# Kernel optimization log

Measured on AMD Instinct MI355X. Metric: run time of the kernel, lower is better.

Reference implementation:

```python
import jax, jax.numpy as jnp
import numpy as np

EPS = 1e-6
FEAT = 1024
HEADS = 16
HDIM = FEAT // HEADS
FF = 500


def setup_inputs() -> dict:
    key = jax.random.key(0)
    ks = jax.random.split(key, 12)
    B, S = 4, 2048
    inp = {
        "x": jax.random.normal(ks[0], (B, S, FEAT), jnp.float32),
        "mask": jax.random.randint(ks[1], (B, S, S), 0, 2, jnp.int32),
        "alpha1": jnp.ones((FEAT,), jnp.float32),
        "bias1": jnp.zeros((FEAT,), jnp.float32),
        "alpha2": jnp.ones((FEAT,), jnp.float32),
        "bias2": jnp.zeros((FEAT,), jnp.float32),
        "Wq": jax.random.normal(ks[2], (FEAT, FEAT), jnp.float32) * (1.0 / np.sqrt(FEAT)),
        "bq": jnp.zeros((FEAT,), jnp.float32),
        "Wk": jax.random.normal(ks[3], (FEAT, FEAT), jnp.float32) * (1.0 / np.sqrt(FEAT)),
        "bk": jnp.zeros((FEAT,), jnp.float32),
        "Wv": jax.random.normal(ks[4], (FEAT, FEAT), jnp.float32) * (1.0 / np.sqrt(FEAT)),
        "bv": jnp.zeros((FEAT,), jnp.float32),
        "Wo": jax.random.normal(ks[5], (FEAT, FEAT), jnp.float32) * (1.0 / np.sqrt(FEAT)),
        "bo": jnp.zeros((FEAT,), jnp.float32),
        "W1": jax.random.normal(ks[6], (FEAT, FF), jnp.float32) * (1.0 / np.sqrt(FEAT)),
        "b1": jnp.zeros((FF,), jnp.float32),
        "W2": jax.random.normal(ks[7], (FF, FEAT), jnp.float32) * (1.0 / np.sqrt(FF)),
        "b2": jnp.zeros((FEAT,), jnp.float32),
    }
    return inp


def _norm(x, alpha, bias):
    m = jnp.mean(x, axis=-1, keepdims=True)
    # torch.std uses Bessel's correction (ddof=1)
    s = jnp.std(x, axis=-1, keepdims=True, ddof=1)
    return alpha * (x - m) / (s + EPS) + bias


def _attn(x2, mask, Wq, bq, Wk, bk, Wv, bv, Wo, bo):
    B, S, _ = x2.shape
    q = (x2 @ Wq + bq).reshape(B, S, HEADS, HDIM)
    k = (x2 @ Wk + bk).reshape(B, S, HEADS, HDIM)
    v = (x2 @ Wv + bv).reshape(B, S, HEADS, HDIM)
    scores = jnp.einsum("bqhd,bkhd->bhqk", q, k) / np.sqrt(HDIM).astype(np.float32)
    # faithful to source: masked positions filled with -1e-09 (not -1e9)
    scores = jnp.where(mask[:, None, :, :] == 0, jnp.float32(-1e-09), scores)
    probs = jax.nn.softmax(scores, axis=-1)
    out = jnp.einsum("bhqk,bkhd->bqhd", probs, v).reshape(B, S, FEAT)
    return out @ Wo + bo


def reference(x, mask, alpha1, bias1, alpha2, bias2, Wq, bq, Wk, bk, Wv, bv, Wo, bo, W1, b1, W2, b2):
    x2 = _norm(x, alpha1, bias1)
    x = x + _attn(x2, mask, Wq, bq, Wk, bk, Wv, bv, Wo, bo)
    x2 = _norm(x, alpha2, bias2)
    h = jax.nn.elu(x2 @ W1 + b1)
    x = x + (h @ W2 + b2)
    return x
```

## Files before the change

kernel.cpp:

```cpp
#include <hip/hip_runtime.h>
#include <hip/hip_bf16.h>
#include <math.h>

#define BATCH 4
#define SEQ 2048
#define FEAT 1024
#define HEADS 16
#define HDIM 64
#define FF 500
#define FFP 512
#define ROWS (BATCH * SEQ)
#define QKVSTR 3072
#define AQ 128

typedef unsigned short ushortT;
typedef __attribute__((ext_vector_type(8))) short short8;
typedef __attribute__((ext_vector_type(4))) float floatx4;

#if defined(__has_builtin) && __has_builtin(__builtin_amdgcn_exp2f)
#define EXP2F(x) __builtin_amdgcn_exp2f(x)
#else
#define EXP2F(x) exp2f(x)
#endif

__device__ __forceinline__ unsigned short f2bf(float f) {
    unsigned int u = __builtin_bit_cast(unsigned int, f);
    u += 0x7fffu + ((u >> 16) & 1u);
    return (unsigned short)(u >> 16);
}
__device__ __forceinline__ float bf2f(short b) {
    unsigned int u = ((unsigned int)(unsigned short)b) << 16;
    return __builtin_bit_cast(float, u);
}

__device__ __forceinline__ void async16(void* lds, const void* g) {
    __builtin_amdgcn_global_load_lds(
        (const __attribute__((address_space(1))) unsigned int*)g,
        (__attribute__((address_space(3))) unsigned int*)lds, 16, 0, 0);
}

__global__ void prep_kernel(const float* __restrict__ Wq, const float* __restrict__ Wk,
                            const float* __restrict__ Wv, const float* __restrict__ Wo,
                            const float* __restrict__ W1, const float* __restrict__ W2,
                            const float* __restrict__ bq, const float* __restrict__ bk,
                            const float* __restrict__ bv, const float* __restrict__ b1,
                            ushortT* __restrict__ Wqkvt, ushortT* __restrict__ Wot,
                            ushortT* __restrict__ W1t, ushortT* __restrict__ W2t,
                            float* __restrict__ bqkv, float* __restrict__ b1p)
{
    const int t = blockIdx.x;
    const int tid = threadIdx.x;
    if (t == 1280) {
        for (int i = tid; i < QKVSTR; i += 256)
            bqkv[i] = (i < 1024) ? bq[i] : ((i < 2048) ? bk[i - 1024] : bv[i - 2048]);
        for (int i = tid; i < FFP; i += 256)
            b1p[i] = (i < FF) ? b1[i] : 0.0f;
        return;
    }
    const float* W; ushortT* Wt; int K, N, Kp, bx, by;
    if (t < 1024) {
        const int wi = t >> 8, lt = t & 255;
        bx = lt & 15; by = lt >> 4; K = FEAT; N = FEAT; Kp = FEAT;
        W  = (wi == 0) ? Wq : (wi == 1) ? Wk : (wi == 2) ? Wv : Wo;
        Wt = (wi == 3) ? Wot : (Wqkvt + (size_t)wi * FEAT * FEAT);
    } else if (t < 1152) {
        const int lt = t - 1024; bx = lt & 7; by = lt >> 3;
        K = FEAT; N = FF; Kp = FEAT; W = W1; Wt = W1t;
    } else {
        const int lt = t - 1152; bx = lt & 15; by = lt >> 4;
        K = FF; N = FEAT; Kp = FFP; W = W2; Wt = W2t;
    }

    __shared__ float T[64][65];
    const int n0 = bx * 64, k0 = by * 64;
    const int r = tid >> 4;
    const int c = (tid & 15) * 4;
    #pragma unroll
    for (int i = 0; i < 4; i++) {
        const int kk = k0 + r + i * 16;
        #pragma unroll
        for (int e = 0; e < 4; e++) {
            const int nn = n0 + c + e;
            T[r + i * 16][c + e] = (kk < K && nn < N) ? W[(size_t)kk * N + nn] : 0.0f;
        }
    }
    __syncthreads();
    #pragma unroll
    for (int i = 0; i < 4; i++) {
        const int nn = r + i * 16;
        if (n0 + nn >= N && Kp == FEAT && N == FF) continue;
        ushort4 o;
        o.x = f2bf(T[c + 0][nn]);
        o.y = f2bf(T[c + 1][nn]);
        o.z = f2bf(T[c + 2][nn]);
        o.w = f2bf(T[c + 3][nn]);
        *(ushort4*)(Wt + (size_t)(n0 + nn) * Kp + k0 + c) = o;
    }
}

__global__ void maskbits_kernel(const int* __restrict__ mask,
                                unsigned int* __restrict__ bits)
{
    const size_t g = (size_t)blockIdx.x * 256 + threadIdx.x;
    const int lane = threadIdx.x & 63;
    const unsigned long long bal = __ballot(mask[g] != 0);
    if (lane == 0)  bits[g >> 5] = (unsigned int)bal;
    if (lane == 32) bits[g >> 5] = (unsigned int)(bal >> 32);
}

__global__ void ln_kernel(const float* __restrict__ x,
                          const float* __restrict__ alpha,
                          const float* __restrict__ bias,
                          ushortT* __restrict__ out)
{
    __shared__ float p1[4], p2[4];
    const int row = blockIdx.x;
    const int tid = threadIdx.x;
    const int wave = tid >> 6, lane = tid & 63;
    float4 v = ((const float4*)(x + (size_t)row * FEAT))[tid];

    float s1 = v.x + v.y + v.z + v.w;
    float s2 = v.x * v.x + v.y * v.y + v.z * v.z + v.w * v.w;
    #pragma unroll
    for (int off = 32; off > 0; off >>= 1) {
        s1 += __shfl_xor(s1, off);
        s2 += __shfl_xor(s2, off);
    }
    if (lane == 0) { p1[wave] = s1; p2[wave] = s2; }
    __syncthreads();
    const float t1 = p1[0] + p1[1] + p1[2] + p1[3];
    const float t2 = p2[0] + p2[1] + p2[2] + p2[3];
    const float mean = t1 * (1.0f / 1024.0f);
    const float var = fmaxf(t2 - 1024.0f * mean * mean, 0.0f) * (1.0f / 1023.0f);
    const float inv = 1.0f / (sqrtf(var) + 1e-6f);

    const float4 a = ((const float4*)alpha)[tid];
    const float4 b = ((const float4*)bias)[tid];
    ushort4 o;
    o.x = f2bf(a.x * (v.x - mean) * inv + b.x);
    o.y = f2bf(a.y * (v.y - mean) * inv + b.y);
    o.z = f2bf(a.z * (v.z - mean) * inv + b.z);
    o.w = f2bf(a.w * (v.w - mean) * inv + b.w);
    ((ushort4*)(out + (size_t)row * FEAT))[tid] = o;
}

template<int ACT, int RES, int OUT_BF16, int BN>
__global__ __launch_bounds__(256)
void mfma_gemm(const ushortT* __restrict__ A, const ushortT* __restrict__ Bt,
               const float* __restrict__ bias, const float* __restrict__ R,
               void* __restrict__ Cout, int M, int N, int K)
{
    constexpr int MT = (BN == 128) ? 4 : 2;
    constexpr int MSPAN = (BN == 128) ? 64 : 32;
    __shared__ ushortT As[2][128 * 32];
    __shared__ ushortT Bs[2][BN * 32];

    const int tid  = threadIdx.x;
    const int wave = tid >> 6, lane = tid & 63;
    const int quad = lane >> 4, l16 = lane & 15;
    const int wm = (BN == 128) ? (wave >> 1) : wave;
    const int wn = (BN == 128) ? (wave & 1) : 0;
    const int row0 = blockIdx.y * 128, col0 = blockIdx.x * BN;

    const floatx4 z4 = {0.f, 0.f, 0.f, 0.f};
    floatx4 acc[MT][4];
    #pragma unroll
    for (int i = 0; i < MT; i++)
        #pragma unroll
        for (int j = 0; j < 4; j++) acc[i][j] = z4;

    for (int k0 = 0; k0 < K; k0 += 64) {
        __syncthreads();
        #pragma unroll
        for (int kh = 0; kh < 2; kh++) {
            #pragma unroll
            for (int i = 0; i < 2; i++) {
                const int rbase = 16 * (wave + 4 * i);
                const int r = rbase + (lane >> 2);
                const int co = (lane & 3) * 8;
                async16((char*)As[kh] + rbase * 64,
                        A + (size_t)(row0 + r) * K + k0 + kh * 32 + co);
            }
            if (BN == 128) {
                #pragma unroll
                for (int i = 0; i < 2; i++) {
                    const int rbase = 16 * (wave + 4 * i);
                    const int r = rbase + (lane >> 2);
                    const int co = (lane & 3) * 8;
                    async16((char*)Bs[kh] + rbase * 64,
                            Bt + (size_t)(col0 + r) * K + k0 + kh * 32 + co);
                }
            } else {
                const int rbase = 16 * wave;
                const int r = rbase + (lane >> 2);
                const int co = (lane & 3) * 8;
                async16((char*)Bs[kh] + rbase * 64,
                        Bt + (size_t)(col0 + r) * K + k0 + kh * 32 + co);
            }
        }
        __syncthreads();

        #pragma unroll
        for (int kh = 0; kh < 2; kh++) {
            short8 af[MT], bf[4];
            #pragma unroll
            for (int mt = 0; mt < MT; mt++)
                af[mt] = *(const short8*)&As[kh][(MSPAN * wm + 16 * mt + l16) * 32 + quad * 8];
            #pragma unroll
            for (int nt = 0; nt < 4; nt++)
                bf[nt] = *(const short8*)&Bs[kh][(64 * wn + 16 * nt + l16) * 32 + quad * 8];
            #pragma unroll
            for (int mt = 0; mt < MT; mt++)
                #pragma unroll
                for (int nt = 0; nt < 4; nt++)
                    acc[mt][nt] = __builtin_amdgcn_mfma_f32_16x16x32_bf16(
                        af[mt], bf[nt], acc[mt][nt], 0, 0, 0);
        }
    }

    #pragma unroll
    for (int mt = 0; mt < MT; mt++) {
        #pragma unroll
        for (int nt = 0; nt < 4; nt++) {
            const int col = col0 + 64 * wn + 16 * nt + l16;
            #pragma unroll
            for (int r = 0; r < 4; r++) {
                const int row = row0 + MSPAN * wm + 16 * mt + quad * 4 + r;
                float val = acc[mt][nt][r] + bias[col];
                if (ACT == 1) val = (val > 0.0f) ? val : (__expf(val) - 1.0f);
                if (RES) val += R[(size_t)row * N + col];
                if (OUT_BF16)
                    ((ushortT*)Cout)[(size_t)row * N + col] = f2bf(val);
                else
                    ((float*)Cout)[(size_t)row * N + col] = val;
            }
        }
    }
}

__global__ void transpose_v_kernel(const ushortT* __restrict__ v, ushortT* __restrict__ vt)
{
    __shared__ ushortT T[64][80];
    const int bid = blockIdx.x;
    const int jt = bid & 31, h = (bid >> 5) & 15, b = bid >> 9;
    const int j0 = jt * 64;
    const int tid = threadIdx.x;

    const int j = tid >> 2;
    #pragma unroll
    for (int i = 0; i < 2; i++) {
        const int c = (tid & 3) * 2 + i;
        short8 val = *(const short8*)(v + (size_t)(b * SEQ + j0 + j) * QKVSTR + h * 64 + c * 8);
        *(short8*)&T[j][c * 8] = val;
    }
    __syncthreads();
    const int d = tid >> 2;
    #pragma unroll
    for (int i = 0; i < 2; i++) {
        const int cj = (tid & 3) * 2 + i;
        union { short8 v8; ushortT u[8]; } tmp;
        #pragma unroll
        for (int e = 0; e < 8; e++) tmp.u[e] = T[cj * 8 + e][d];
        *(short8*)(vt + ((size_t)((b * HEADS + h) * 64 + d)) * SEQ + j0 + cj * 8) = tmp.v8;
    }
}

__global__ __launch_bounds__(256)
void mfma_attn(const ushortT* __restrict__ qkv, const ushortT* __restrict__ vt,
               const unsigned int* __restrict__ mbits, ushortT* __restrict__ attn_out)
{
    __shared__ ushortT Ks[2][64 * 64];
    __shared__ ushortT Vts[2][64 * 64];
    __shared__ ushortT Ps[AQ * 64];

    const int tid = threadIdx.x;
    const int wave = tid >> 6, lane = tid & 63;
    const int quad = lane >> 4, l16 = lane & 15;
    const int bid = blockIdx.x;
    const int qt = bid & 15, h = (bid >> 4) & 15, b = bid >> 8;
    const int q0 = qt * AQ;

    const ushortT* qptr = qkv;
    const ushortT* kptr = qkv + 1024;

    short8 qf[2][2];
    #pragma unroll
    for (int mg = 0; mg < 2; mg++) {
        const size_t qrow = (size_t)(b * SEQ + q0 + 32 * wave + mg * 16 + l16);
        short8 t0 = *(const short8*)(qptr + qrow * QKVSTR + h * 64 + quad * 8);
        short8 t1 = *(const short8*)(qptr + qrow * QKVSTR + h * 64 + 32 + quad * 8);
        const float cs = 0.125f * 1.4426950408889634f;
        #pragma unroll
        for (int i = 0; i < 8; i++) {
            qf[mg][0][i] = (short)f2bf(bf2f(t0[i]) * cs);
            qf[mg][1][i] = (short)f2bf(bf2f(t1[i]) * cs);
        }
    }

    short8 ones8;
    #pragma unroll
    for (int i = 0; i < 8; i++) ones8[i] = (short)0x3F80;

    const floatx4 z4 = {0.f, 0.f, 0.f, 0.f};
    floatx4 o[2][4];
    #pragma unroll
    for (int mg = 0; mg < 2; mg++)
        #pragma unroll
        for (int dt = 0; dt < 4; dt++) o[mg][dt] = z4;
    floatx4 lacc[2] = {z4, z4};

    const int rr = tid >> 2;
    const int c0 = (tid & 3) * 2;
    const ushortT* gk = kptr + (size_t)(b * SEQ + rr) * QKVSTR + h * 64;
    const ushortT* gv = vt + ((size_t)((b * HEADS + h) * 64 + rr)) * SEQ;
    short8 rk0, rk1, rv0, rv1;

#define ATTN_ISSUE() {                                                       \
    rk0 = *(const short8*)(gk + c0 * 8);                                     \
    rk1 = *(const short8*)(gk + c0 * 8 + 8);                                 \
    rv0 = *(const short8*)(gv + c0 * 8);                                     \
    rv1 = *(const short8*)(gv + c0 * 8 + 8);                                 \
    gk += (size_t)64 * QKVSTR; gv += 64; }

#define ATTN_WRITE(BI) {                                                     \
    *(short8*)&Ks[BI][rr * 64 + ((c0 ^ (rr & 7)) * 8)] = rk0;                \
    *(short8*)&Ks[BI][rr * 64 + (((c0 + 1) ^ (rr & 7)) * 8)] = rk1;          \
    *(short8*)&Vts[BI][rr * 64 + ((c0 ^ (rr & 7)) * 8)] = rv0;               \
    *(short8*)&Vts[BI][rr * 64 + (((c0 + 1) ^ (rr & 7)) * 8)] = rv1; }

    const unsigned int* mrowp[2];
    mrowp[0] = mbits + (size_t)(b * SEQ + q0 + 32 * wave + l16) * (SEQ / 32);
    mrowp[1] = mrowp[0] + 16 * (SEQ / 32);
    const int mloc0 = 32 * wave + l16;

    ATTN_ISSUE();
    ATTN_WRITE(0);

    #pragma unroll 2
    for (int jt = 0; jt < 32; jt++) {
        __syncthreads();
        const int cur = jt & 1;
        unsigned int w[2][2];
        #pragma unroll
        for (int mg = 0; mg < 2; mg++) {
            w[mg][0] = mrowp[mg][jt * 2];
            w[mg][1] = mrowp[mg][jt * 2 + 1];
        }
        if (jt < 31) ATTN_ISSUE();

        floatx4 st[2][4];
        #pragma unroll
        for (int nt = 0; nt < 4; nt++) {
            const int j = nt * 16 + l16;
            short8 ka0 = *(const short8*)&Ks[cur][j * 64 + ((quad ^ (j & 7)) * 8)];
            short8 ka1 = *(const short8*)&Ks[cur][j * 64 + (((4 + quad) ^ (j & 7)) * 8)];
            #pragma unroll
            for (int mg = 0; mg < 2; mg++) {
                floatx4 t = z4;
                t = __builtin_amdgcn_mfma_f32_16x16x32_bf16(ka0, qf[mg][0], t, 0, 0, 0);
                t = __builtin_amdgcn_mfma_f32_16x16x32_bf16(ka1, qf[mg][1], t, 0, 0, 0);
                st[mg][nt] = t;
            }
        }

        #pragma unroll
        for (int mg = 0; mg < 2; mg++) {
            const int mloc = mloc0 + mg * 16;
            #pragma unroll
            for (int nt = 0; nt < 4; nt++) {
                const unsigned int ww = (nt & 2) ? w[mg][1] : w[mg][0];
                const unsigned int wsh = ww >> ((nt & 1) * 16 + quad * 4);
                float p[4];
                p[0] = EXP2F((wsh & 1u) ? st[mg][nt][0] : 0.0f);
                p[1] = EXP2F((wsh & 2u) ? st[mg][nt][1] : 0.0f);
                p[2] = EXP2F((wsh & 4u) ? st[mg][nt][2] : 0.0f);
                p[3] = EXP2F((wsh & 8u) ? st[mg][nt][3] : 0.0f);
                const int j0 = nt * 16 + quad * 4;
                const int chunk = (j0 >> 3) ^ (mloc & 7);
                const int ci = j0 & 7;
                ushortT* dst = &Ps[mloc * 64 + chunk * 8 + ci];
                *(__hip_bfloat162*)(dst)     = __float22bfloat162_rn(make_float2(p[0], p[1]));
                *(__hip_bfloat162*)(dst + 2) = __float22bfloat162_rn(make_float2(p[2], p[3]));
            }
        }

        short8 pa[2][2];
        #pragma unroll
        for (int mg = 0; mg < 2; mg++) {
            const int mloc = mloc0 + mg * 16;
            pa[mg][0] = *(const short8*)&Ps[mloc * 64 + ((quad ^ (mloc & 7)) * 8)];
            pa[mg][1] = *(const short8*)&Ps[mloc * 64 + (((4 + quad) ^ (mloc & 7)) * 8)];
            lacc[mg] = __builtin_amdgcn_mfma_f32_16x16x32_bf16(pa[mg][0], ones8, lacc[mg], 0, 0, 0);
            lacc[mg] = __builtin_amdgcn_mfma_f32_16x16x32_bf16(pa[mg][1], ones8, lacc[mg], 0, 0, 0);
        }
        #pragma unroll
        for (int dt = 0; dt < 4; dt++) {
            const int d = dt * 16 + l16;
            short8 vb0 = *(const short8*)&Vts[cur][d * 64 + ((quad ^ (d & 7)) * 8)];
            short8 vb1 = *(const short8*)&Vts[cur][d * 64 + (((4 + quad) ^ (d & 7)) * 8)];
            #pragma unroll
            for (int mg = 0; mg < 2; mg++) {
                o[mg][dt] = __builtin_amdgcn_mfma_f32_16x16x32_bf16(pa[mg][0], vb0, o[mg][dt], 0, 0, 0);
                o[mg][dt] = __builtin_amdgcn_mfma_f32_16x16x32_bf16(pa[mg][1], vb1, o[mg][dt], 0, 0, 0);
            }
        }

        if (jt < 31) ATTN_WRITE(cur ^ 1);
    }

    #pragma unroll
    for (int mg = 0; mg < 2; mg++) {
        #pragma unroll
        for (int r = 0; r < 4; r++) {
            const float inv_l = 1.0f / lacc[mg][r];
            const size_t row = (size_t)(b * SEQ + q0 + 32 * wave + mg * 16 + quad * 4 + r);
            #pragma unroll
            for (int dt = 0; dt < 4; dt++) {
                attn_out[row * FEAT + h * 64 + dt * 16 + l16] = f2bf(o[mg][dt][r] * inv_l);
            }
        }
    }
#undef ATTN_ISSUE
#undef ATTN_WRITE
}

extern "C" void kernel_launch(void* const* d_in, const int* in_sizes, int n_in,
                              void* d_out, int out_size, void* d_ws, size_t ws_size,
                              hipStream_t stream)
{
    const float* x      = (const float*)d_in[0];
    const int*   mask   = (const int*)d_in[1];
    const float* alpha1 = (const float*)d_in[2];
    const float* bias1  = (const float*)d_in[3];
    const float* alpha2 = (const float*)d_in[4];
    const float* bias2  = (const float*)d_in[5];
    const float* Wq     = (const float*)d_in[6];
    const float* bq     = (const float*)d_in[7];
    const float* Wk     = (const float*)d_in[8];
    const float* bk     = (const float*)d_in[9];
    const float* Wv     = (const float*)d_in[10];
    const float* bv     = (const float*)d_in[11];
    const float* Wo     = (const float*)d_in[12];
    const float* bo     = (const float*)d_in[13];
    const float* W1     = (const float*)d_in[14];
    const float* b1     = (const float*)d_in[15];
    const float* W2     = (const float*)d_in[16];
    const float* b2     = (const float*)d_in[17];
    float* out = (float*)d_out;

    char* ws = (char*)d_ws;
    const size_t MB = 1024 * 1024;
    ushortT* x2b    = (ushortT*)(ws);
    ushortT* attn_o = (ushortT*)(ws);
    ushortT* qkv    = (ushortT*)(ws + 16 * MB);
    ushortT* x2b2   = (ushortT*)(ws + 16 * MB);
    ushortT* hbuf   = (ushortT*)(ws + 32 * MB);
    ushortT* vtb    = (ushortT*)(ws + 64 * MB);
    ushortT* Wqkvt  = (ushortT*)(ws + 80 * MB);
    ushortT* Wot    = (ushortT*)(ws + 86 * MB);
    ushortT* W1t    = (ushortT*)(ws + 88 * MB);
    ushortT* W2t    = (ushortT*)(ws + 89 * MB);
    float*   b1p    = (float*)  (ws + 90 * MB);
    float*   bqkv   = (float*)  (ws + 90 * MB + 16384);
    unsigned int* mbits = (unsigned int*)(ws + 91 * MB);

    const dim3 blk(256);

    prep_kernel<<<1281, blk, 0, stream>>>(Wq, Wk, Wv, Wo, W1, W2, bq, bk, bv, b1,
                                          Wqkvt, Wot, W1t, W2t, bqkv, b1p);
    maskbits_kernel<<<(BATCH * SEQ * SEQ) / 256, blk, 0, stream>>>(mask, mbits);

    ln_kernel<<<ROWS, blk, 0, stream>>>(x, alpha1, bias1, x2b);

    mfma_gemm<0, 0, 1, 128><<<dim3(24, 64), blk, 0, stream>>>(
        x2b, Wqkvt, bqkv, nullptr, qkv, ROWS, QKVSTR, FEAT);

    transpose_v_kernel<<<BATCH * HEADS * (SEQ / 64), blk, 0, stream>>>(qkv + 2048, vtb);
    mfma_attn<<<BATCH * HEADS * (SEQ / AQ), blk, 0, stream>>>(qkv, vtb, mbits, attn_o);

    mfma_gemm<0, 1, 0, 128><<<dim3(8, 64), blk, 0, stream>>>(
        attn_o, Wot, bo, x, out, ROWS, FEAT, FEAT);

    ln_kernel<<<ROWS, blk, 0, stream>>>(out, alpha2, bias2, x2b2);

    mfma_gemm<1, 0, 1, 64><<<dim3(FFP / 64, 64), blk, 0, stream>>>(
        x2b2, W1t, b1p, nullptr, hbuf, ROWS, FFP, FEAT);

    mfma_gemm<0, 1, 0, 128><<<dim3(8, 64), blk, 0, stream>>>(
        hbuf, W2t, b2, out, out, ROWS, FEAT, FFP);
}
```

Baseline: 473.4 us.

## Fuse V transpose into QKV GEMM epilogue, remap GEMM blocks per XCD, single-buffer attention LDS

The QKV GEMM now writes Q and K to a narrower 2048-stride buffer and writes V straight into the head-transposed layout from its epilogue, so the separate transpose kernel and its round trip through memory go away. All GEMMs switch to a 1D grid with a block-index remap that groups column tiles by XCD, aiming for better L2 reuse of the weight tiles. The attention kernel drops its double-buffered K/V shared-memory tiles in favour of a single buffer with an extra barrier, which lowers LDS use but serializes the store with compute. The skip of padded rows in the weight prep kernel is also removed. The transposed V stores are only 8-byte scattered writes, which may be less efficient than the old transpose kernel's writes.

New measurement: 483.5 us. 2.1% more time.

```diff
diff --git a/kernel.cpp b/kernel.cpp
--- a/kernel.cpp
+++ b/kernel.cpp
@@ -11,6 +11,7 @@
 #define FFP 512
 #define ROWS (BATCH * SEQ)
 #define QKVSTR 3072
+#define QKSTR 2048
 #define AQ 128
 
 typedef unsigned short ushortT;
@@ -88,7 +89,6 @@
     #pragma unroll
     for (int i = 0; i < 4; i++) {
         const int nn = r + i * 16;
-        if (n0 + nn >= N && Kp == FEAT && N == FF) continue;
         ushort4 o;
         o.x = f2bf(T[c + 0][nn]);
         o.y = f2bf(T[c + 1][nn]);
@@ -144,14 +144,16 @@
     ((ushort4*)(out + (size_t)row * FEAT))[tid] = o;
 }
 
-template<int ACT, int RES, int OUT_BF16, int BN>
+template<int ACT, int RES, int OUT_BF16, int BN, int TNX, int SPLITV>
 __global__ __launch_bounds__(256)
 void mfma_gemm(const ushortT* __restrict__ A, const ushortT* __restrict__ Bt,
                const float* __restrict__ bias, const float* __restrict__ R,
-               void* __restrict__ Cout, int M, int N, int K)
+               void* __restrict__ Cout, ushortT* __restrict__ vtout,
+               int M, int N, int K)
 {
     constexpr int MT = (BN == 128) ? 4 : 2;
     constexpr int MSPAN = (BN == 128) ? 64 : 32;
+    constexpr int CPX = TNX >> 3;
     __shared__ ushortT As[2][128 * 32];
     __shared__ ushortT Bs[2][BN * 32];
 
@@ -160,7 +162,12 @@
     const int quad = lane >> 4, l16 = lane & 15;
     const int wm = (BN == 128) ? (wave >> 1) : wave;
     const int wn = (BN == 128) ? (wave & 1) : 0;
-    const int row0 = blockIdx.y * 128, col0 = blockIdx.x * BN;
+
+    const int id = blockIdx.x;
+    const int xcd = id & 7, s = id >> 3;
+    const int bx = xcd * CPX + (s % CPX);
+    const int by = s / CPX;
+    const int row0 = by * 128, col0 = bx * BN;
 
     const floatx4 z4 = {0.f, 0.f, 0.f, 0.f};
     floatx4 acc[MT][4];
@@ -218,6 +225,29 @@
         }
     }
 
+    if (SPLITV && col0 >= 2048) {
+        #pragma unroll
+        for (int mt = 0; mt < MT; mt++) {
+            const int row = row0 + MSPAN * wm + 16 * mt + quad * 4;
+            const int b = row >> 11, j = row & (SEQ - 1);
+            #pragma unroll
+            for (int nt = 0; nt < 4; nt++) {
+                const int col = col0 + 64 * wn + 16 * nt + l16;
+                const int cv = col - 2048;
+                const int h = cv >> 6, d = cv & 63;
+                const float bb = bias[col];
+                ushort4 o;
+                o.x = f2bf(acc[mt][nt][0] + bb);
+                o.y = f2bf(acc[mt][nt][1] + bb);
+                o.z = f2bf(acc[mt][nt][2] + bb);
+                o.w = f2bf(acc[mt][nt][3] + bb);
+                *(ushort4*)(vtout + ((size_t)((b * HEADS + h) * 64 + d)) * SEQ + j) = o;
+            }
+        }
+        return;
+    }
+
+    const int cn = SPLITV ? QKSTR : N;
     #pragma unroll
     for (int mt = 0; mt < MT; mt++) {
         #pragma unroll
@@ -230,47 +260,20 @@
                 if (ACT == 1) val = (val > 0.0f) ? val : (__expf(val) - 1.0f);
                 if (RES) val += R[(size_t)row * N + col];
                 if (OUT_BF16)
-                    ((ushortT*)Cout)[(size_t)row * N + col] = f2bf(val);
+                    ((ushortT*)Cout)[(size_t)row * cn + col] = f2bf(val);
                 else
-                    ((float*)Cout)[(size_t)row * N + col] = val;
-            }
-        }
-    }
-}
-
-__global__ void transpose_v_kernel(const ushortT* __restrict__ v, ushortT* __restrict__ vt)
-{
-    __shared__ ushortT T[64][80];
-    const int bid = blockIdx.x;
-    const int jt = bid & 31, h = (bid >> 5) & 15, b = bid >> 9;
-    const int j0 = jt * 64;
-    const int tid = threadIdx.x;
-
-    const int j = tid >> 2;
-    #pragma unroll
-    for (int i = 0; i < 2; i++) {
-        const int c = (tid & 3) * 2 + i;
-        short8 val = *(const short8*)(v + (size_t)(b * SEQ + j0 + j) * QKVSTR + h * 64 + c * 8);
-        *(short8*)&T[j][c * 8] = val;
-    }
-    __syncthreads();
-    const int d = tid >> 2;
-    #pragma unroll
-    for (int i = 0; i < 2; i++) {
-        const int cj = (tid & 3) * 2 + i;
-        union { short8 v8; ushortT u[8]; } tmp;
-        #pragma unroll
-        for (int e = 0; e < 8; e++) tmp.u[e] = T[cj * 8 + e][d];
-        *(short8*)(vt + ((size_t)((b * HEADS + h) * 64 + d)) * SEQ + j0 + cj * 8) = tmp.v8;
+                    ((float*)Cout)[(size_t)row * cn + col] = val;
+            }
+        }
     }
 }
 
 __global__ __launch_bounds__(256)
-void mfma_attn(const ushortT* __restrict__ qkv, const ushortT* __restrict__ vt,
+void mfma_attn(const ushortT* __restrict__ qk, const ushortT* __restrict__ vt,
                const unsigned int* __restrict__ mbits, ushortT* __restrict__ attn_out)
 {
-    __shared__ ushortT Ks[2][64 * 64];
-    __shared__ ushortT Vts[2][64 * 64];
+    __shared__ ushortT Ks[64 * 64];
+    __shared__ ushortT Vts[64 * 64];
     __shared__ ushortT Ps[AQ * 64];
 
     const int tid = threadIdx.x;
@@ -280,15 +283,15 @@
     const int qt = bid & 15, h = (bid >> 4) & 15, b = bid >> 8;
     const int q0 = qt * AQ;
 
-    const ushortT* qptr = qkv;
-    const ushortT* kptr = qkv + 1024;
+    const ushortT* qptr = qk;
+    const ushortT* kptr = qk + 1024;
 
     short8 qf[2][2];
     #pragma unroll
     for (int mg = 0; mg < 2; mg++) {
         const size_t qrow = (size_t)(b * SEQ + q0 + 32 * wave + mg * 16 + l16);
-        short8 t0 = *(const short8*)(qptr + qrow * QKVSTR + h * 64 + quad * 8);
-        short8 t1 = *(const short8*)(qptr + qrow * QKVSTR + h * 64 + 32 + quad * 8);
+        short8 t0 = *(const short8*)(qptr + qrow * QKSTR + h * 64 + quad * 8);
+        short8 t1 = *(const short8*)(qptr + qrow * QKSTR + h * 64 + 32 + quad * 8);
         const float cs = 0.125f * 1.4426950408889634f;
         #pragma unroll
         for (int i = 0; i < 8; i++) {
@@ -311,7 +314,7 @@
 
     const int rr = tid >> 2;
     const int c0 = (tid & 3) * 2;
-    const ushortT* gk = kptr + (size_t)(b * SEQ + rr) * QKVSTR + h * 64;
+    const ushortT* gk = kptr + (size_t)(b * SEQ + rr) * QKSTR + h * 64;
     const ushortT* gv = vt + ((size_t)((b * HEADS + h) * 64 + rr)) * SEQ;
     short8 rk0, rk1, rv0, rv1;
 
@@ -320,13 +323,13 @@
     rk1 = *(const short8*)(gk + c0 * 8 + 8);                                 \
     rv0 = *(const short8*)(gv + c0 * 8);                                     \
     rv1 = *(const short8*)(gv + c0 * 8 + 8);                                 \
-    gk += (size_t)64 * QKVSTR; gv += 64; }
-
-#define ATTN_WRITE(BI) {                                                     \
-    *(short8*)&Ks[BI][rr * 64 + ((c0 ^ (rr & 7)) * 8)] = rk0;                \
-    *(short8*)&Ks[BI][rr * 64 + (((c0 + 1) ^ (rr & 7)) * 8)] = rk1;          \
-    *(short8*)&Vts[BI][rr * 64 + ((c0 ^ (rr & 7)) * 8)] = rv0;               \
-    *(short8*)&Vts[BI][rr * 64 + (((c0 + 1) ^ (rr & 7)) * 8)] = rv1; }
+    gk += (size_t)64 * QKSTR; gv += 64; }
+
+#define ATTN_WRITE() {                                                       \
+    *(short8*)&Ks[rr * 64 + ((c0 ^ (rr & 7)) * 8)] = rk0;                    \
+    *(short8*)&Ks[rr * 64 + (((c0 + 1) ^ (rr & 7)) * 8)] = rk1;              \
+    *(short8*)&Vts[rr * 64 + ((c0 ^ (rr & 7)) * 8)] = rv0;                   \
+    *(short8*)&Vts[rr * 64 + (((c0 + 1) ^ (rr & 7)) * 8)] = rv1; }
 
     const unsigned int* mrowp[2];
     mrowp[0] = mbits + (size_t)(b * SEQ + q0 + 32 * wave + l16) * (SEQ / 32);
@@ -334,12 +337,10 @@
     const int mloc0 = 32 * wave + l16;
 
     ATTN_ISSUE();
-    ATTN_WRITE(0);
-
-    #pragma unroll 2
+    ATTN_WRITE();
+
     for (int jt = 0; jt < 32; jt++) {
         __syncthreads();
-        const int cur = jt & 1;
         unsigned int w[2][2];
         #pragma unroll
         for (int mg = 0; mg < 2; mg++) {
@@ -352,8 +353,8 @@
         #pragma unroll
         for (int nt = 0; nt < 4; nt++) {
             const int j = nt * 16 + l16;
-            short8 ka0 = *(const short8*)&Ks[cur][j * 64 + ((quad ^ (j & 7)) * 8)];
-            short8 ka1 = *(const short8*)&Ks[cur][j * 64 + (((4 + quad) ^ (j & 7)) * 8)];
+            short8 ka0 = *(const short8*)&Ks[j * 64 + ((quad ^ (j & 7)) * 8)];
+            short8 ka1 = *(const short8*)&Ks[j * 64 + (((4 + quad) ^ (j & 7)) * 8)];
             #pragma unroll
             for (int mg = 0; mg < 2; mg++) {
                 floatx4 t = z4;
@@ -396,8 +397,8 @@
         #pragma unroll
         for (int dt = 0; dt < 4; dt++) {
             const int d = dt * 16 + l16;
-            short8 vb0 = *(const short8*)&Vts[cur][d * 64 + ((quad ^ (d & 7)) * 8)];
-            short8 vb1 = *(const short8*)&Vts[cur][d * 64 + (((4 + quad) ^ (d & 7)) * 8)];
+            short8 vb0 = *(const short8*)&Vts[d * 64 + ((quad ^ (d & 7)) * 8)];
+            short8 vb1 = *(const short8*)&Vts[d * 64 + (((4 + quad) ^ (d & 7)) * 8)];
             #pragma unroll
             for (int mg = 0; mg < 2; mg++) {
                 o[mg][dt] = __builtin_amdgcn_mfma_f32_16x16x32_bf16(pa[mg][0], vb0, o[mg][dt], 0, 0, 0);
@@ -405,7 +406,8 @@
             }
         }
 
-        if (jt < 31) ATTN_WRITE(cur ^ 1);
+        __syncthreads();
+        if (jt < 31) ATTN_WRITE();
     }
 
     #pragma unroll
@@ -452,10 +454,10 @@
     const size_t MB = 1024 * 1024;
     ushortT* x2b    = (ushortT*)(ws);
     ushortT* attn_o = (ushortT*)(ws);
-    ushortT* qkv    = (ushortT*)(ws + 16 * MB);
+    ushortT* qk     = (ushortT*)(ws + 16 * MB);
     ushortT* x2b2   = (ushortT*)(ws + 16 * MB);
     ushortT* hbuf   = (ushortT*)(ws + 32 * MB);
-    ushortT* vtb    = (ushortT*)(ws + 64 * MB);
+    ushortT* vtb    = (ushortT*)(ws + 48 * MB);
     ushortT* Wqkvt  = (ushortT*)(ws + 80 * MB);
     ushortT* Wot    = (ushortT*)(ws + 86 * MB);
     ushortT* W1t    = (ushortT*)(ws + 88 * MB);
@@ -472,20 +474,19 @@
 
     ln_kernel<<<ROWS, blk, 0, stream>>>(x, alpha1, bias1, x2b);
 
-    mfma_gemm<0, 0, 1, 128><<<dim3(24, 64), blk, 0, stream>>>(
-        x2b, Wqkvt, bqkv, nullptr, qkv, ROWS, QKVSTR, FEAT);
-
-    transpose_v_kernel<<<BATCH * HEADS * (SEQ / 64), blk, 0, stream>>>(qkv + 2048, vtb);
-    mfma_attn<<<BATCH * HEADS * (SEQ / AQ), blk, 0, stream>>>(qkv, vtb, mbits, attn_o);
-
-    mfma_gemm<0, 1, 0, 128><<<dim3(8, 64), blk, 0, stream>>>(
-        attn_o, Wot, bo, x, out, ROWS, FEAT, FEAT);
+    mfma_gemm<0, 0, 1, 128, 24, 1><<<1536, blk, 0, stream>>>(
+        x2b, Wqkvt, bqkv, nullptr, qk, vtb, ROWS, QKVSTR, FEAT);
+
+    mfma_attn<<<BATCH * HEADS * (SEQ / AQ), blk, 0, stream>>>(qk, vtb, mbits, attn_o);
+
+    mfma_gemm<0, 1, 0, 128, 8, 0><<<512, blk, 0, stream>>>(
+        attn_o, Wot, bo, x, out, nullptr, ROWS, FEAT, FEAT);
 
     ln_kernel<<<ROWS, blk, 0, stream>>>(out, alpha2, bias2, x2b2);
 
-    mfma_gemm<1, 0, 1, 64><<<dim3(FFP / 64, 64), blk, 0, stream>>>(
-        x2b2, W1t, b1p, nullptr, hbuf, ROWS, FFP, FEAT);
-
-    mfma_gemm<0, 1, 0, 128><<<dim3(8, 64), blk, 0, stream>>>(
-        hbuf, W2t, b2, out, out, ROWS, FEAT, FFP);
-}
+    mfma_gemm<1, 0, 1, 64, 8, 0><<<512, blk, 0, stream>>>(
+        x2b2, W1t, b1p, nullptr, hbuf, nullptr, ROWS, FFP, FEAT);
+
+    mfma_gemm<0, 1, 0, 128, 8, 0><<<512, blk, 0, stream>>>(
+        hbuf, W2t, b2, out, out, nullptr, ROWS, FEAT, FFP);
+}
```
